# Optimization experiments

Measured on AMD Instinct MI355X. Metric: run time of the kernel, lower is better.

The kernel has to match this reference:

```python
import jax, jax.numpy as jnp
import numpy as np


def setup_inputs() -> dict:
    key = jax.random.key(0)
    ks = jax.random.split(key, 5)
    B, c_in, c_out, style_d = 8, 128, 128, 512
    D = H = W = 32
    f = 3
    # xavier_uniform-like scale for conv weight
    fan_in = c_in * f * f * f
    fan_out = c_out * f * f * f
    limit = float(np.sqrt(6.0 / (fan_in + fan_out)))
    x = jax.random.normal(ks[0], (B, c_in, D, H, W), dtype=jnp.float32)
    s = jax.random.normal(ks[1], (B, style_d), dtype=jnp.float32)
    w = jax.random.uniform(ks[2], (c_out, c_in, f, f, f), dtype=jnp.float32, minval=-limit, maxval=limit)
    b = jnp.zeros((c_out, 1, 1, 1), dtype=jnp.float32)
    lim_a = float(np.sqrt(1.0 / style_d))
    affine_w = jax.random.uniform(ks[3], (c_in, style_d), dtype=jnp.float32, minval=-lim_a, maxval=lim_a)
    affine_b = jnp.zeros((c_in,), dtype=jnp.float32)
    return {"x": x, "s": s, "w": w, "b": b, "affine_w": affine_w, "affine_b": affine_b}


def _per_sample_conv(xi, wi):
    # xi: [c_in, D, H, W], wi: [c_out, c_in, 3, 3, 3]
    out = jax.lax.conv_general_dilated(
        xi[None],  # [1, c_in, D, H, W]
        wi,
        window_strides=(1, 1, 1),
        padding=((1, 1), (1, 1), (1, 1)),
        dimension_numbers=("NCDHW", "OIDHW", "NCDHW"),
    )
    return out[0]  # [c_out, D, H, W]


def reference(x, s, w, b, affine_w, affine_b):
    # Style -> per-sample channel scales
    style = s @ affine_w.T + affine_b  # [B, c_in]
    # Modulate: [B, c_out, c_in, f, f, f]
    wmod = w[None] * (style[:, None, :, None, None, None] + 1.0)
    # Demodulate
    d = jnp.sqrt(jnp.sum(jnp.square(wmod), axis=(2, 3, 4, 5), keepdims=True) + 1e-8)
    wmod = wmod / d
    # Per-sample conv (equivalent to grouped conv with groups=B)
    out = jax.vmap(_per_sample_conv)(x, wmod)  # [B, c_out, D, H, W]
    return out + b[None]
```

## Files before the change

kernel.cpp:

```cpp
#include <hip/hip_runtime.h>
#include <stdint.h>
#include <stddef.h>

typedef __attribute__((ext_vector_type(8))) short short8;
typedef __attribute__((ext_vector_type(4))) float floatx4;

#define CI 128
#define CO 128
#define SP 32768
#define BATCH 8
#define STYLED 512
#define KV 3456

typedef __attribute__((address_space(1))) const void gvoid_t;
typedef __attribute__((address_space(3))) void lvoid_t;

__device__ __forceinline__ void gload16(const void* g, void* l) {
    __builtin_amdgcn_global_load_lds((gvoid_t*)g, (lvoid_t*)l, 16, 0, 0);
}

__device__ __forceinline__ short f2bf(float f) {
    uint32_t u = __builtin_bit_cast(uint32_t, f);
    u = (u + 0x7FFFu + ((u >> 16) & 1u)) >> 16;
    return (short)(u & 0xFFFFu);
}

__global__ void k_style(const float* __restrict__ s, const float* __restrict__ aw,
                        const float* __restrict__ ab, float* __restrict__ m) {
    __shared__ float ssh[STYLED];
    int b = blockIdx.x;
    int i = threadIdx.x;
    for (int r = 0; r < STYLED / 128; ++r) ssh[r * 128 + i] = s[b * STYLED + r * 128 + i];
    __syncthreads();
    float acc = ab[i] + 1.0f;
    const float4* awr = (const float4*)(aw + (size_t)i * STYLED);
    for (int d4 = 0; d4 < STYLED / 4; ++d4) {
        float4 v = awr[d4];
        acc += v.x * ssh[d4 * 4] + v.y * ssh[d4 * 4 + 1] + v.z * ssh[d4 * 4 + 2] + v.w * ssh[d4 * 4 + 3];
    }
    m[b * CI + i] = acc;
}

__global__ void k_wmod(const float* __restrict__ w, const float* __restrict__ m,
                       short* __restrict__ wt) {
    int b = blockIdx.x >> 7;
    int o = blockIdx.x & 127;
    int lane = threadIdx.x;
    const float* wrow = w + (size_t)o * KV;
    const float* mrow = m + b * CI;
    float sum = 0.f;
    for (int e = lane; e < KV; e += 64) {
        int i = e / 27;
        float v = wrow[e] * mrow[i];
        sum += v * v;
    }
    #pragma unroll
    for (int off = 32; off >= 1; off >>= 1) sum += __shfl_xor(sum, off);
    float scale = 1.0f / sqrtf(sum + 1e-8f);
    int ophase = (o >> 1) & 3;
    for (int e = lane; e < KV; e += 64) {
        int i = e / 27;
        int k = e - i * 27;
        float v = wrow[e] * mrow[i] * scale;
        int c = i >> 5, il = i & 31, g = il >> 3, r = il & 7;
        int gl = g ^ ophase;
        wt[(((size_t)((b * 4 + c) * 27 + k)) * 128 + o) * 32 + gl * 8 + r] = f2bf(v);
    }
}

__global__ void k_xt(const float* __restrict__ x, short* __restrict__ xt) {
    __shared__ short t[128 * 130 + 2];
    int bid = blockIdx.x;
    int b = bid >> 8;
    int z = (bid >> 3) & 31;
    int y0 = (bid & 7) * 4;
    int tid = threadIdx.x;
    const float* src = x + (size_t)b * CI * SP + (size_t)z * 1024 + (size_t)y0 * 32;
    int r8 = tid >> 5;
    int s32 = tid & 31;
    for (int it = 0; it < 16; ++it) {
        int ch = it * 8 + r8;
        float4 v = *(const float4*)(src + (size_t)ch * SP + s32 * 4);
        uint32_t p0 = ((uint32_t)(uint16_t)f2bf(v.y) << 16) | (uint16_t)f2bf(v.x);
        uint32_t p1 = ((uint32_t)(uint16_t)f2bf(v.w) << 16) | (uint16_t)f2bf(v.z);
        uint32_t* row = (uint32_t*)&t[ch * 130 + s32 * 4];
        row[0] = p0;
        row[1] = p1;
    }
    __syncthreads();
    short* dstb = xt + ((size_t)(b * SP + z * 1024 + y0 * 32)) * CI;
    for (int it = 0; it < 8; ++it) {
        int idx = it * 256 + tid;
        int sp = idx >> 4, g = idx & 15;
        short8 v;
        #pragma unroll
        for (int j = 0; j < 8; ++j) v[j] = t[(g * 8 + j) * 130 + sp];
        *(short8*)(dstb + (size_t)sp * CI + g * 8) = v;
    }
}

__launch_bounds__(512, 4)
__global__ void k_conv(const short* __restrict__ xt, const short* __restrict__ wt,
                       const float* __restrict__ bias, float* __restrict__ out,
                       const short* __restrict__ zeropage) {
    __shared__ short lds_x[816 * 32];
    __shared__ short lds_w0[128 * 32];
    __shared__ short lds_w1[128 * 32];
    __shared__ short lds_w2[128 * 32];

    int bid = blockIdx.x;
    int b = bid & 7;
    int t = bid >> 3;
    int zt = t & 15, yt = t >> 4;
    int z0 = zt * 2, y0 = yt * 4;

    int tid = threadIdx.x;
    int lane = tid & 63;
    int wid = tid >> 6;
    int wm = wid >> 2;
    int wn = wid & 3;
    int l15 = lane & 15;
    int lhi = lane >> 4;

    floatx4 acc[4][4];
    #pragma unroll
    for (int a = 0; a < 4; ++a)
        #pragma unroll
        for (int c = 0; c < 4; ++c) acc[a][c] = (floatx4){0.f, 0.f, 0.f, 0.f};

    const short* wb = wt + (size_t)b * (4 * 27 * 128 * 32);
    const short* xb = xt + (size_t)b * SP * CI;

    for (int c = 0; c < 4; ++c) {
        for (int j = 0; ; ++j) {
            int s = wid + 8 * j;
            if (s >= 51) break;
            int G = s * 64 + lane;
            int rowid = G >> 2, g = G & 3;
            int zh = rowid / 204; int rr = rowid - zh * 204;
            int yh = rr / 34;     int wh = rr - yh * 34;
            int zz = z0 + zh - 1, yy = y0 + yh - 1, ww = wh - 1;
            int q = g ^ ((rowid >> 1) & 3);
            const short* src;
            if ((unsigned)zz < 32u && (unsigned)yy < 32u && (unsigned)ww < 32u)
                src = xb + ((size_t)(zz * 1024 + yy * 32 + ww)) * CI + c * 32 + q * 8;
            else
                src = zeropage + q * 8;
            gload16(src, (void*)((char*)lds_x + s * 1024));
        }
        gload16(wb + ((size_t)(c * 27 + 0)) * 4096 + wid * 512 + lane * 8,
                (void*)((char*)lds_w0 + wid * 1024));
        gload16(wb + ((size_t)(c * 27 + 1)) * 4096 + wid * 512 + lane * 8,
                (void*)((char*)lds_w1 + wid * 1024));
        asm volatile("s_waitcnt vmcnt(1)" ::: "memory");
        __builtin_amdgcn_s_barrier();
        asm volatile("" ::: "memory");

        short* wcur = lds_w0;
        short* wnx1 = lds_w1;
        short* wnx2 = lds_w2;

        for (int tap = 0; tap < 27; ++tap) {
            if (tap < 25)
                gload16(wb + ((size_t)(c * 27 + tap + 2)) * 4096 + wid * 512 + lane * 8,
                        (void*)((char*)wnx2 + wid * 1024));
            int kd = tap / 9, r9 = tap - kd * 9;
            int kh = r9 / 3, kw = r9 - kh * 3;

            short8 af[4];
            #pragma unroll
            for (int mf = 0; mf < 4; ++mf) {
                int o = wm * 64 + mf * 16 + l15;
                af[mf] = *(const short8*)((const char*)wcur + o * 64 +
                                          ((lhi ^ ((o >> 1) & 3)) << 4));
            }
            #pragma unroll
            for (int nf = 0; nf < 4; ++nf) {
                int n = wn * 64 + nf * 16;
                int zi = n >> 7, yi = (n >> 5) & 3;
                int h = ((zi + kd) * 6 + (yi + kh)) * 34 + (n & 31) + kw + l15;
                short8 bf = *(const short8*)((const char*)lds_x + h * 64 +
                                             ((lhi ^ ((h >> 1) & 3)) << 4));
                #pragma unroll
                for (int mf = 0; mf < 4; ++mf)
                    acc[mf][nf] = __builtin_amdgcn_mfma_f32_16x16x32_bf16(af[mf], bf, acc[mf][nf], 0, 0, 0);
            }

            if (tap < 25)       asm volatile("s_waitcnt vmcnt(1)" ::: "memory");
            else if (tap == 25) asm volatile("s_waitcnt vmcnt(0)" ::: "memory");
            __builtin_amdgcn_s_barrier();
            asm volatile("" ::: "memory");

            short* tmp = wcur; wcur = wnx1; wnx1 = wnx2; wnx2 = tmp;
        }
    }

    float bv[4][4];
    #pragma unroll
    for (int mf = 0; mf < 4; ++mf)
        #pragma unroll
        for (int j = 0; j < 4; ++j)
            bv[mf][j] = bias[wm * 64 + mf * 16 + lhi * 4 + j];

    #pragma unroll
    for (int mf = 0; mf < 4; ++mf) {
        int o = wm * 64 + mf * 16 + lhi * 4;
        #pragma unroll
        for (int nf = 0; nf < 4; ++nf) {
            int n = wn * 64 + nf * 16;
            int zi = n >> 7, yi = (n >> 5) & 3, wcol = (n & 31) + l15;
            size_t obase = ((size_t)(b * CO + o)) * SP + (size_t)(z0 + zi) * 1024 + (y0 + yi) * 32 + wcol;
            #pragma unroll
            for (int j = 0; j < 4; ++j)
                out[obase + (size_t)j * SP] = acc[mf][nf][j] + bv[mf][j];
        }
    }
}

extern "C" void kernel_launch(void* const* d_in, const int* in_sizes, int n_in,
                              void* d_out, int out_size, void* d_ws, size_t ws_size,
                              hipStream_t stream) {
    const float* x  = (const float*)d_in[0];
    const float* s  = (const float*)d_in[1];
    const float* w  = (const float*)d_in[2];
    const float* bb = (const float*)d_in[3];
    const float* aw = (const float*)d_in[4];
    const float* ab = (const float*)d_in[5];
    float* out = (float*)d_out;

    float* style_m = (float*)d_ws;
    short* wmodT   = (short*)((char*)d_ws + 4096);
    short* xT      = (short*)((char*)d_ws + 4096 + 7077888);
    short* zpage   = (short*)((char*)d_ws + 4096 + 7077888 + 67108864);

    hipMemsetAsync(zpage, 0, 256, stream);
    k_style<<<BATCH, 128, 0, stream>>>(s, aw, ab, style_m);
    k_wmod<<<BATCH * CO, 64, 0, stream>>>(w, style_m, wmodT);
    k_xt<<<BATCH * 32 * 8, 256, 0, stream>>>(x, xT);
    k_conv<<<BATCH * 128, 512, 0, stream>>>(xT, wmodT, bb, out, zpage);
}
```

Baseline: 297.5 us.

## Prefetch weight fragments into registers, simplify transpose, fold zero-page memset

The conv inner loop now loads the activation fragments first, then issues the weight prefetch. It also reads the next tap's weight fragments into double-buffered registers before the MFMAs and raises wave priority around the MFMA block, so the LDS read latency can overlap with compute. The input transpose kernel drops its LDS staging and has each thread read 32 channels directly and write 64 contiguous bytes. The zero-page memset is folded into the style kernel, removing one launch. Risks are higher register pressure from the fully unrolled tap loop and uncoalesced-ish strided reads in the transpose.

```diff
diff --git a/kernel.cpp b/kernel.cpp
--- a/kernel.cpp
+++ b/kernel.cpp
@@ -14,7 +14,6 @@
 
 typedef __attribute__((address_space(1))) const void gvoid_t;
 typedef __attribute__((address_space(3))) void lvoid_t;
-
 __device__ __forceinline__ void gload16(const void* g, void* l) {
     __builtin_amdgcn_global_load_lds((gvoid_t*)g, (lvoid_t*)l, 16, 0, 0);
 }
@@ -26,10 +25,12 @@
 }
 
 __global__ void k_style(const float* __restrict__ s, const float* __restrict__ aw,
-                        const float* __restrict__ ab, float* __restrict__ m) {
+                        const float* __restrict__ ab, float* __restrict__ m,
+                        float* __restrict__ zp) {
     __shared__ float ssh[STYLED];
     int b = blockIdx.x;
     int i = threadIdx.x;
+    if (b == 0 && i < 64) zp[i] = 0.f;
     for (int r = 0; r < STYLED / 128; ++r) ssh[r * 128 + i] = s[b * STYLED + r * 128 + i];
     __syncthreads();
     float acc = ab[i] + 1.0f;
@@ -69,40 +70,27 @@
 }
 
 __global__ void k_xt(const float* __restrict__ x, short* __restrict__ xt) {
-    __shared__ short t[128 * 130 + 2];
     int bid = blockIdx.x;
-    int b = bid >> 8;
-    int z = (bid >> 3) & 31;
-    int y0 = (bid & 7) * 4;
-    int tid = threadIdx.x;
-    const float* src = x + (size_t)b * CI * SP + (size_t)z * 1024 + (size_t)y0 * 32;
-    int r8 = tid >> 5;
-    int s32 = tid & 31;
-    for (int it = 0; it < 16; ++it) {
-        int ch = it * 8 + r8;
-        float4 v = *(const float4*)(src + (size_t)ch * SP + s32 * 4);
-        uint32_t p0 = ((uint32_t)(uint16_t)f2bf(v.y) << 16) | (uint16_t)f2bf(v.x);
-        uint32_t p1 = ((uint32_t)(uint16_t)f2bf(v.w) << 16) | (uint16_t)f2bf(v.z);
-        uint32_t* row = (uint32_t*)&t[ch * 130 + s32 * 4];
-        row[0] = p0;
-        row[1] = p1;
-    }
-    __syncthreads();
-    short* dstb = xt + ((size_t)(b * SP + z * 1024 + y0 * 32)) * CI;
-    for (int it = 0; it < 8; ++it) {
-        int idx = it * 256 + tid;
-        int sp = idx >> 4, g = idx & 15;
-        short8 v;
-        #pragma unroll
-        for (int j = 0; j < 8; ++j) v[j] = t[(g * 8 + j) * 130 + sp];
-        *(short8*)(dstb + (size_t)sp * CI + g * 8) = v;
-    }
+    int b = bid >> 9, c = (bid >> 7) & 3, spb = bid & 127;
+    int sp = spb * 256 + threadIdx.x;
+    const float* src = x + ((size_t)(b * CI + c * 32)) * SP + sp;
+    float f[32];
+    #pragma unroll
+    for (int ch = 0; ch < 32; ++ch) f[ch] = src[(size_t)ch * SP];
+    short8 v[4];
+    #pragma unroll
+    for (int q = 0; q < 4; ++q)
+        #pragma unroll
+        for (int j = 0; j < 8; ++j) v[q][j] = f2bf(f[q * 8 + j]);
+    short* dst = xt + (size_t)(b * SP + sp) * CI + c * 32;
+    #pragma unroll
+    for (int q = 0; q < 4; ++q) *(short8*)(dst + q * 8) = v[q];
 }
 
 __launch_bounds__(512, 4)
 __global__ void k_conv(const short* __restrict__ xt, const short* __restrict__ wt,
                        const float* __restrict__ bias, float* __restrict__ out,
-                       const short* __restrict__ zeropage) {
+                       const short* __restrict__ zp) {
     __shared__ short lds_x[816 * 32];
     __shared__ short lds_w0[128 * 32];
     __shared__ short lds_w1[128 * 32];
@@ -110,8 +98,8 @@
 
     int bid = blockIdx.x;
     int b = bid & 7;
-    int t = bid >> 3;
-    int zt = t & 15, yt = t >> 4;
+    int t0 = bid >> 3;
+    int zt = t0 & 15, yt = t0 >> 4;
     int z0 = zt * 2, y0 = yt * 4;
 
     int tid = threadIdx.x;
@@ -131,7 +119,11 @@
     const short* wb = wt + (size_t)b * (4 * 27 * 128 * 32);
     const short* xb = xt + (size_t)b * SP * CI;
 
+    short* const wbuf[3] = {lds_w0, lds_w1, lds_w2};
+
+    #pragma unroll 1
     for (int c = 0; c < 4; ++c) {
+        __syncthreads();
         for (int j = 0; ; ++j) {
             int s = wid + 8 * j;
             if (s >= 51) break;
@@ -145,53 +137,78 @@
             if ((unsigned)zz < 32u && (unsigned)yy < 32u && (unsigned)ww < 32u)
                 src = xb + ((size_t)(zz * 1024 + yy * 32 + ww)) * CI + c * 32 + q * 8;
             else
-                src = zeropage + q * 8;
+                src = zp + q * 8;
             gload16(src, (void*)((char*)lds_x + s * 1024));
         }
-        gload16(wb + ((size_t)(c * 27 + 0)) * 4096 + wid * 512 + lane * 8,
+        const short* wbc = wb + (size_t)c * 27 * 4096;
+        gload16(wbc + (size_t)0 * 4096 + wid * 512 + lane * 8,
                 (void*)((char*)lds_w0 + wid * 1024));
-        gload16(wb + ((size_t)(c * 27 + 1)) * 4096 + wid * 512 + lane * 8,
+        gload16(wbc + (size_t)1 * 4096 + wid * 512 + lane * 8,
                 (void*)((char*)lds_w1 + wid * 1024));
         asm volatile("s_waitcnt vmcnt(1)" ::: "memory");
         __builtin_amdgcn_s_barrier();
         asm volatile("" ::: "memory");
 
-        short* wcur = lds_w0;
-        short* wnx1 = lds_w1;
-        short* wnx2 = lds_w2;
-
+        short8 afA[4], afB[4];
+        #pragma unroll
+        for (int mf = 0; mf < 4; ++mf) {
+            int o = wm * 64 + mf * 16 + l15;
+            afA[mf] = *(const short8*)((const char*)lds_w0 + o * 64 +
+                                       ((lhi ^ ((o >> 1) & 3)) << 4));
+        }
+
+        #pragma unroll
         for (int tap = 0; tap < 27; ++tap) {
-            if (tap < 25)
-                gload16(wb + ((size_t)(c * 27 + tap + 2)) * 4096 + wid * 512 + lane * 8,
-                        (void*)((char*)wnx2 + wid * 1024));
             int kd = tap / 9, r9 = tap - kd * 9;
             int kh = r9 / 3, kw = r9 - kh * 3;
 
-            short8 af[4];
-            #pragma unroll
-            for (int mf = 0; mf < 4; ++mf) {
-                int o = wm * 64 + mf * 16 + l15;
-                af[mf] = *(const short8*)((const char*)wcur + o * 64 +
-                                          ((lhi ^ ((o >> 1) & 3)) << 4));
-            }
+            short8 xf[4];
             #pragma unroll
             for (int nf = 0; nf < 4; ++nf) {
                 int n = wn * 64 + nf * 16;
                 int zi = n >> 7, yi = (n >> 5) & 3;
                 int h = ((zi + kd) * 6 + (yi + kh)) * 34 + (n & 31) + kw + l15;
-                short8 bf = *(const short8*)((const char*)lds_x + h * 64 +
-                                             ((lhi ^ ((h >> 1) & 3)) << 4));
+                xf[nf] = *(const short8*)((const char*)lds_x + h * 64 +
+                                          ((lhi ^ ((h >> 1) & 3)) << 4));
+            }
+
+            if (tap < 25)
+                gload16(wbc + (size_t)(tap + 2) * 4096 + wid * 512 + lane * 8,
+                        (void*)((char*)wbuf[(tap + 2) % 3] + wid * 1024));
+
+            if (tap < 26) {
+                if (tap < 25) asm volatile("s_waitcnt vmcnt(1)" ::: "memory");
+                else          asm volatile("s_waitcnt vmcnt(0)" ::: "memory");
+                __builtin_amdgcn_s_barrier();
+                asm volatile("" ::: "memory");
+                const short* wnext = wbuf[(tap + 1) % 3];
+                if ((tap & 1) == 0) {
+                    #pragma unroll
+                    for (int mf = 0; mf < 4; ++mf) {
+                        int o = wm * 64 + mf * 16 + l15;
+                        afB[mf] = *(const short8*)((const char*)wnext + o * 64 +
+                                                   ((lhi ^ ((o >> 1) & 3)) << 4));
+                    }
+                } else {
+                    #pragma unroll
+                    for (int mf = 0; mf < 4; ++mf) {
+                        int o = wm * 64 + mf * 16 + l15;
+                        afA[mf] = *(const short8*)((const char*)wnext + o * 64 +
+                                                   ((lhi ^ ((o >> 1) & 3)) << 4));
+                    }
+                }
+            }
+
+            __builtin_amdgcn_s_setprio(1);
+            #pragma unroll
+            for (int nf = 0; nf < 4; ++nf) {
                 #pragma unroll
-                for (int mf = 0; mf < 4; ++mf)
-                    acc[mf][nf] = __builtin_amdgcn_mfma_f32_16x16x32_bf16(af[mf], bf, acc[mf][nf], 0, 0, 0);
+                for (int mf = 0; mf < 4; ++mf) {
+                    acc[mf][nf] = __builtin_amdgcn_mfma_f32_16x16x32_bf16(
+                        ((tap & 1) == 0) ? afA[mf] : afB[mf], xf[nf], acc[mf][nf], 0, 0, 0);
+                }
             }
-
-            if (tap < 25)       asm volatile("s_waitcnt vmcnt(1)" ::: "memory");
-            else if (tap == 25) asm volatile("s_waitcnt vmcnt(0)" ::: "memory");
-            __builtin_amdgcn_s_barrier();
-            asm volatile("" ::: "memory");
-
-            short* tmp = wcur; wcur = wnx1; wnx1 = wnx2; wnx2 = tmp;
+            __builtin_amdgcn_s_setprio(0);
         }
     }
 
@@ -231,11 +248,10 @@
     float* style_m = (float*)d_ws;
     short* wmodT   = (short*)((char*)d_ws + 4096);
     short* xT      = (short*)((char*)d_ws + 4096 + 7077888);
-    short* zpage   = (short*)((char*)d_ws + 4096 + 7077888 + 67108864);
-
-    hipMemsetAsync(zpage, 0, 256, stream);
-    k_style<<<BATCH, 128, 0, stream>>>(s, aw, ab, style_m);
+    float* zpage   = (float*)((char*)d_ws + 4096 + 7077888 + 67108864);
+
+    k_style<<<BATCH, 128, 0, stream>>>(s, aw, ab, style_m, zpage);
     k_wmod<<<BATCH * CO, 64, 0, stream>>>(w, style_m, wmodT);
-    k_xt<<<BATCH * 32 * 8, 256, 0, stream>>>(x, xT);
-    k_conv<<<BATCH * 128, 512, 0, stream>>>(xT, wmodT, bb, out, zpage);
-}
+    k_xt<<<BATCH * 4 * 128, 256, 0, stream>>>(x, xT);
+    k_conv<<<BATCH * 128, 512, 0, stream>>>(xT, wmodT, bb, out, (const short*)zpage);
+}
```

New measurement: 489.3 us. +64.5%, slower.
